# Kernel tuning notes

Hardware: AMD Instinct MI355X
Metric: run time of the kernel (lower is better)

## Reference

```python
import jax, jax.numpy as jnp
import numpy as np

N_EMITTERS = 200000
N_FRAMES = 500


def setup_inputs() -> dict:
    key = jax.random.key(0)
    k1, _ = jax.random.split(key)
    # initial state must be one-hot per emitter: column 0 = 'on', column 1 = 'off'
    on = jax.random.bernoulli(k1, 0.5, (N_EMITTERS,))
    initial = jnp.stack([on, ~on], axis=-1).astype(jnp.float32)  # [N, 2] one-hot
    # transition[j] is the categorical distribution over {stay-ish, flip-ish} given row j
    transition = jnp.array([[0.5, 0.5], [0.9, 0.1]], dtype=jnp.float32)
    # transition_matrix[0] = identity (keep state), transition_matrix[1] = swap (flip state)
    transition_matrix = jnp.array([[[1.0, 0.0], [0.0, 1.0]],
                                   [[0.0, 1.0], [1.0, 0.0]]], dtype=jnp.float32)
    return {"initial": initial, "transition": transition,
            "transition_matrix": transition_matrix, "n_frames": N_FRAMES}


def reference(initial, transition, transition_matrix, n_frames):
    # Faithful translation of the per-frame Python loop as a single lax.scan.
    # Original: A = Cat(transition).sample([N]) -> A[n, j] ~ Cat(transition[j, :]) in {0, 1}
    #           t = (state * A).sum(-1)   (selects A at the current one-hot state index)
    #           state = state @ transition_matrix[t]
    # Output: per-frame on-mask (original returned np.where(state[:, 0] == 1) indices,
    # which has data-dependent shape; we return the equivalent dense mask).
    p1 = transition[:, 1]  # prob of drawing class 1 for each of the 2 row-distributions
    keys = jax.random.split(jax.random.key(42), n_frames)

    def step(state, k):
        u = jax.random.uniform(k, (state.shape[0], 2), dtype=state.dtype)  # [N, 2]
        A = (u < p1[None, :]).astype(state.dtype)  # categorical sample per row dist, {0,1}
        t = jnp.sum(state * A, axis=-1).astype(jnp.int32)  # [N] chosen action per emitter
        m = transition_matrix[t]  # [N, 2, 2] identity-or-swap
        new_state = jnp.einsum('ni,nij->nj', state, m)  # [N, 2] one-hot update
        return new_state, new_state[:, 0]

    _, on_mask = jax.lax.scan(step, initial, keys)
    return on_mask  # [n_frames, N], 1.0 where emitter is in the 'on' state
```

## Files before the change

### kernel.cpp

```cpp
#include <hip/hip_runtime.h>
#include <stdint.h>


#define ROTL32(x, d) __builtin_amdgcn_alignbit((x), (x), 32 - (d))

typedef uint32_t v2u __attribute__((ext_vector_type(2)));

__device__ __forceinline__ void tf2x32(uint32_t k0, uint32_t k1,
                                       uint32_t x0, uint32_t x1,
                                       uint32_t& o0, uint32_t& o1) {
  const uint32_t k2 = k0 ^ k1 ^ 0x1BD11BDAu;
  x0 += k0; x1 += k1;
#define TF_R(d) { x0 += x1; x1 = ROTL32(x1, d) ^ x0; }
  TF_R(13) TF_R(15) TF_R(26) TF_R(6)
  x0 += k1; x1 += k2 + 1u;
  TF_R(17) TF_R(29) TF_R(16) TF_R(24)
  x0 += k2; x1 += k0 + 2u;
  TF_R(13) TF_R(15) TF_R(26) TF_R(6)
  x0 += k0; x1 += k1 + 3u;
  TF_R(17) TF_R(29) TF_R(16) TF_R(24)
  x0 += k1; x1 += k2 + 4u;
  TF_R(13) TF_R(15) TF_R(26) TF_R(6)
  x0 += k2; x1 += k0 + 5u;
#undef TF_R
  o0 = x0; o1 = x1;
}

__global__ void subkeys_kernel(uint2* __restrict__ ks, int nf, int cap) {
  const int f = blockIdx.x * blockDim.x + threadIdx.x;
  if (f < nf) {
    uint32_t a, b;
    tf2x32(0u, 42u, 0u, (uint32_t)f, a, b);
    ks[f] = make_uint2(a, b);
  } else if (f < cap) {
    ks[f] = make_uint2(0u, 0u);
  }
}

__device__ __forceinline__ v2u do_frame(
    uint32_t k0, uint32_t k1, uint32_t& sA, uint32_t& sB,
    uint32_t& thrA, uint32_t& thrB, uint32_t baseA, uint32_t baseB,
    uint32_t tsh0, uint32_t tsh1, uint32_t sw0, uint32_t sw1) {
  const uint32_t k2 = k0 ^ k1 ^ 0x1BD11BDAu;
  const uint32_t c1 = k2 + 1u, c2 = k0 + 2u, c3 = k1 + 3u,
                 c4 = k2 + 4u, c5 = k0 + 5u;

  uint32_t xa0 = k0, xa1 = baseA + sA + k1;
  uint32_t xb0 = k0, xb1 = baseB + sB + k1;

#define RND(d) { xa0 += xa1; xa1 = ROTL32(xa1, (d)) ^ xa0;   \
                 xb0 += xb1; xb1 = ROTL32(xb1, (d)) ^ xb0; }
  RND(13) RND(15) RND(26) RND(6)
  xa0 += k1; xa1 += c1; xb0 += k1; xb1 += c1;
  RND(17) RND(29) RND(16) RND(24)
  xa0 += k2; xa1 += c2; xb0 += k2; xb1 += c2;
  RND(13) RND(15) RND(26) RND(6)
  xa0 += k0; xa1 += c3; xb0 += k0; xb1 += c3;
  RND(17) RND(29) RND(16) RND(24)
  xa0 += k1; xa1 += c4; xb0 += k1; xb1 += c4;
  RND(13) RND(15) RND(26) RND(6)
  xa0 += k2; xa1 += c5; xb0 += k2; xb1 += c5;
#undef RND

  sA ^= ((xa0 ^ xa1) < thrA) ? sw1 : sw0;
  sB ^= ((xb0 ^ xb1) < thrB) ? sw1 : sw0;
  thrA = sA ? tsh1 : tsh0;
  thrB = sB ? tsh1 : tsh0;
  v2u v;
  v.x = sA ? 0u : 0x3f800000u;
  v.y = sB ? 0u : 0x3f800000u;
  return v;
}

__device__ __forceinline__ void markov_body(
    const float* __restrict__ initial, const float* __restrict__ transition,
    const float* __restrict__ tmat, const uint2* __restrict__ ks,
    float* __restrict__ out, int N, int nf) {
  const int t = blockIdx.x * blockDim.x + threadIdx.x;
  const int nA = 2 * t;
  const int nB = 2 * t + 1;
  if (nA >= N) return;
  const bool hasB = (nB < N);

  const uint64_t t0w = ((uint64_t)(uint32_t)ceilf(transition[1] * 8388608.0f)) << 9;
  const uint64_t t1w = ((uint64_t)(uint32_t)ceilf(transition[3] * 8388608.0f)) << 9;
  const uint32_t tsh0 = (t0w > 0xFFFFFFFFull) ? 0xFFFFFFFFu : (uint32_t)t0w;
  const uint32_t tsh1 = (t1w > 0xFFFFFFFFull) ? 0xFFFFFFFFu : (uint32_t)t1w;
  const uint32_t sw0 = (tmat[1] != 0.0f) ? 1u : 0u;
  const uint32_t sw1 = (tmat[5] != 0.0f) ? 1u : 0u;

  uint32_t sA = (initial[2 * nA] != 0.0f) ? 0u : 1u;
  uint32_t sB = hasB ? ((initial[2 * nB] != 0.0f) ? 0u : 1u) : 0u;
  uint32_t thrA = sA ? tsh1 : tsh0;
  uint32_t thrB = sB ? tsh1 : tsh0;
  const uint32_t baseA = 2u * (uint32_t)nA;
  const uint32_t baseB = 2u * (uint32_t)nB;

  float* op = out + nA;
  const uint4* kq = (const uint4*)ks;

  const int ng = nf / 4;
  uint4 a0 = kq[0], a1 = kq[1];
  if (hasB) {
    for (int g = 0; g < ng; ++g) {
      const uint4 b0 = kq[2 * g + 2];
      const uint4 b1 = kq[2 * g + 3];
      const v2u v0 = do_frame(a0.x, a0.y, sA, sB, thrA, thrB, baseA, baseB,
                              tsh0, tsh1, sw0, sw1);
      __builtin_nontemporal_store(v0, (v2u*)op); op += N;
      const v2u v1 = do_frame(a0.z, a0.w, sA, sB, thrA, thrB, baseA, baseB,
                              tsh0, tsh1, sw0, sw1);
      __builtin_nontemporal_store(v1, (v2u*)op); op += N;
      const v2u v2 = do_frame(a1.x, a1.y, sA, sB, thrA, thrB, baseA, baseB,
                              tsh0, tsh1, sw0, sw1);
      __builtin_nontemporal_store(v2, (v2u*)op); op += N;
      const v2u v3 = do_frame(a1.z, a1.w, sA, sB, thrA, thrB, baseA, baseB,
                              tsh0, tsh1, sw0, sw1);
      __builtin_nontemporal_store(v3, (v2u*)op); op += N;
      a0 = b0; a1 = b1;
    }
    for (int f = ng * 4; f < nf; ++f) {
      const uint2 k = ks[f];
      const v2u v = do_frame(k.x, k.y, sA, sB, thrA, thrB, baseA, baseB,
                             tsh0, tsh1, sw0, sw1);
      __builtin_nontemporal_store(v, (v2u*)op); op += N;
    }
  } else {
    for (int f = 0; f < nf; ++f) {
      const uint2 k = ks[f];
      const v2u v = do_frame(k.x, k.y, sA, sB, thrA, thrB, baseA, baseB,
                             tsh0, tsh1, sw0, sw1);
      __builtin_nontemporal_store(v.x, (uint32_t*)op); op += N;
    }
  }
}

__global__ __launch_bounds__(64) void markov_kernel(
    const float* __restrict__ initial, const float* __restrict__ transition,
    const float* __restrict__ tmat, const uint2* __restrict__ ks,
    float* __restrict__ out, int N, int nf) {
  markov_body(initial, transition, tmat, ks, out, N, nf);
}

__global__ __launch_bounds__(64) void markov_kernel_lds(
    const float* __restrict__ initial, const float* __restrict__ transition,
    const float* __restrict__ tmat, float* __restrict__ out,
    int N, int nf, int cap) {
  extern __shared__ uint2 kf[];
  for (int f = threadIdx.x; f < cap; f += blockDim.x) {
    uint2 k = make_uint2(0u, 0u);
    if (f < nf) {
      uint32_t a, b;
      tf2x32(0u, 42u, 0u, (uint32_t)f, a, b);
      k = make_uint2(a, b);
    }
    kf[f] = k;
  }
  __syncthreads();
  markov_body(initial, transition, tmat, kf, out, N, nf);
}

extern "C" void kernel_launch(void* const* d_in, const int* in_sizes, int n_in,
                              void* d_out, int out_size, void* d_ws, size_t ws_size,
                              hipStream_t stream) {
  const float* initial    = (const float*)d_in[0];
  const float* transition = (const float*)d_in[1];
  const float* tmat       = (const float*)d_in[2];
  float* out = (float*)d_out;

  const int N  = in_sizes[0] / 2;
  const int nf = (N > 0) ? (out_size / N) : 0;
  if (N <= 0 || nf <= 0) return;

  const int nthreads = (N + 1) / 2;
  const int block = 64;
  const int grid = (nthreads + block - 1) / block;

  const int cap = (nf / 4 + 2) * 4;
  const size_t need = (size_t)cap * sizeof(uint2);
  if (ws_size >= need) {
    uint2* ks = (uint2*)d_ws;
    subkeys_kernel<<<(cap + 255) / 256, 256, 0, stream>>>(ks, nf, cap);
    markov_kernel<<<grid, block, 0, stream>>>(initial, transition, tmat, ks,
                                              out, N, nf);
  } else {
    markov_kernel_lds<<<grid, block, need, stream>>>(initial, transition,
                                                     tmat, out, N, nf, cap);
  }
}
```

Measured before the change: 261.3 us.

## Process one emitter per thread with 256-thread blocks instead of two per thread

Each thread now handles a single emitter rather than a pair, which doubles the thread count (200k threads) and halves the per-thread ILP from two interleaved Threefry streams to one. Block size goes from 64 to 256 and output stores become 4-byte per lane instead of 8-byte vector stores. The goal is more wavefronts to hide latency and simpler code, at the cost of less per-thread instruction-level parallelism and twice as many subkey loads across the grid.

```diff
diff --git a/kernel.cpp b/kernel.cpp
--- a/kernel.cpp
+++ b/kernel.cpp
@@ -3,8 +3,6 @@
 
 
 #define ROTL32(x, d) __builtin_amdgcn_alignbit((x), (x), 32 - (d))
-
-typedef uint32_t v2u __attribute__((ext_vector_type(2)));
 
 __device__ __forceinline__ void tf2x32(uint32_t k0, uint32_t k1,
                                        uint32_t x0, uint32_t x1,
@@ -37,50 +35,38 @@
   }
 }
 
-__device__ __forceinline__ v2u do_frame(
-    uint32_t k0, uint32_t k1, uint32_t& sA, uint32_t& sB,
-    uint32_t& thrA, uint32_t& thrB, uint32_t baseA, uint32_t baseB,
+__device__ __forceinline__ uint32_t do_frame1(
+    uint32_t k0, uint32_t k1, uint32_t& s, uint32_t& thr, uint32_t base,
     uint32_t tsh0, uint32_t tsh1, uint32_t sw0, uint32_t sw1) {
   const uint32_t k2 = k0 ^ k1 ^ 0x1BD11BDAu;
   const uint32_t c1 = k2 + 1u, c2 = k0 + 2u, c3 = k1 + 3u,
                  c4 = k2 + 4u, c5 = k0 + 5u;
 
-  uint32_t xa0 = k0, xa1 = baseA + sA + k1;
-  uint32_t xb0 = k0, xb1 = baseB + sB + k1;
-
-#define RND(d) { xa0 += xa1; xa1 = ROTL32(xa1, (d)) ^ xa0;   \
-                 xb0 += xb1; xb1 = ROTL32(xb1, (d)) ^ xb0; }
+  uint32_t x0 = k0, x1 = base + s + k1;
+#define RND(d) { x0 += x1; x1 = ROTL32(x1, (d)) ^ x0; }
   RND(13) RND(15) RND(26) RND(6)
-  xa0 += k1; xa1 += c1; xb0 += k1; xb1 += c1;
+  x0 += k1; x1 += c1;
   RND(17) RND(29) RND(16) RND(24)
-  xa0 += k2; xa1 += c2; xb0 += k2; xb1 += c2;
+  x0 += k2; x1 += c2;
   RND(13) RND(15) RND(26) RND(6)
-  xa0 += k0; xa1 += c3; xb0 += k0; xb1 += c3;
+  x0 += k0; x1 += c3;
   RND(17) RND(29) RND(16) RND(24)
-  xa0 += k1; xa1 += c4; xb0 += k1; xb1 += c4;
+  x0 += k1; x1 += c4;
   RND(13) RND(15) RND(26) RND(6)
-  xa0 += k2; xa1 += c5; xb0 += k2; xb1 += c5;
+  x0 += k2; x1 += c5;
 #undef RND
 
-  sA ^= ((xa0 ^ xa1) < thrA) ? sw1 : sw0;
-  sB ^= ((xb0 ^ xb1) < thrB) ? sw1 : sw0;
-  thrA = sA ? tsh1 : tsh0;
-  thrB = sB ? tsh1 : tsh0;
-  v2u v;
-  v.x = sA ? 0u : 0x3f800000u;
-  v.y = sB ? 0u : 0x3f800000u;
-  return v;
+  s ^= ((x0 ^ x1) < thr) ? sw1 : sw0;
+  thr = s ? tsh1 : tsh0;
+  return s ? 0u : 0x3f800000u;
 }
 
 __device__ __forceinline__ void markov_body(
     const float* __restrict__ initial, const float* __restrict__ transition,
     const float* __restrict__ tmat, const uint2* __restrict__ ks,
     float* __restrict__ out, int N, int nf) {
-  const int t = blockIdx.x * blockDim.x + threadIdx.x;
-  const int nA = 2 * t;
-  const int nB = 2 * t + 1;
-  if (nA >= N) return;
-  const bool hasB = (nB < N);
+  const int n = blockIdx.x * blockDim.x + threadIdx.x;
+  if (n >= N) return;
 
   const uint64_t t0w = ((uint64_t)(uint32_t)ceilf(transition[1] * 8388608.0f)) << 9;
   const uint64_t t1w = ((uint64_t)(uint32_t)ceilf(transition[3] * 8388608.0f)) << 9;
@@ -89,60 +75,43 @@
   const uint32_t sw0 = (tmat[1] != 0.0f) ? 1u : 0u;
   const uint32_t sw1 = (tmat[5] != 0.0f) ? 1u : 0u;
 
-  uint32_t sA = (initial[2 * nA] != 0.0f) ? 0u : 1u;
-  uint32_t sB = hasB ? ((initial[2 * nB] != 0.0f) ? 0u : 1u) : 0u;
-  uint32_t thrA = sA ? tsh1 : tsh0;
-  uint32_t thrB = sB ? tsh1 : tsh0;
-  const uint32_t baseA = 2u * (uint32_t)nA;
-  const uint32_t baseB = 2u * (uint32_t)nB;
+  uint32_t s = (initial[2 * n] != 0.0f) ? 0u : 1u;
+  uint32_t thr = s ? tsh1 : tsh0;
+  const uint32_t base = 2u * (uint32_t)n;
 
-  float* op = out + nA;
+  uint32_t* op = (uint32_t*)(out + n);
   const uint4* kq = (const uint4*)ks;
 
   const int ng = nf / 4;
   uint4 a0 = kq[0], a1 = kq[1];
-  if (hasB) {
-    for (int g = 0; g < ng; ++g) {
-      const uint4 b0 = kq[2 * g + 2];
-      const uint4 b1 = kq[2 * g + 3];
-      const v2u v0 = do_frame(a0.x, a0.y, sA, sB, thrA, thrB, baseA, baseB,
-                              tsh0, tsh1, sw0, sw1);
-      __builtin_nontemporal_store(v0, (v2u*)op); op += N;
-      const v2u v1 = do_frame(a0.z, a0.w, sA, sB, thrA, thrB, baseA, baseB,
-                              tsh0, tsh1, sw0, sw1);
-      __builtin_nontemporal_store(v1, (v2u*)op); op += N;
-      const v2u v2 = do_frame(a1.x, a1.y, sA, sB, thrA, thrB, baseA, baseB,
-                              tsh0, tsh1, sw0, sw1);
-      __builtin_nontemporal_store(v2, (v2u*)op); op += N;
-      const v2u v3 = do_frame(a1.z, a1.w, sA, sB, thrA, thrB, baseA, baseB,
-                              tsh0, tsh1, sw0, sw1);
-      __builtin_nontemporal_store(v3, (v2u*)op); op += N;
-      a0 = b0; a1 = b1;
-    }
-    for (int f = ng * 4; f < nf; ++f) {
-      const uint2 k = ks[f];
-      const v2u v = do_frame(k.x, k.y, sA, sB, thrA, thrB, baseA, baseB,
-                             tsh0, tsh1, sw0, sw1);
-      __builtin_nontemporal_store(v, (v2u*)op); op += N;
-    }
-  } else {
-    for (int f = 0; f < nf; ++f) {
-      const uint2 k = ks[f];
-      const v2u v = do_frame(k.x, k.y, sA, sB, thrA, thrB, baseA, baseB,
-                             tsh0, tsh1, sw0, sw1);
-      __builtin_nontemporal_store(v.x, (uint32_t*)op); op += N;
-    }
+  for (int g = 0; g < ng; ++g) {
+    const uint4 b0 = kq[2 * g + 2];
+    const uint4 b1 = kq[2 * g + 3];
+    const uint32_t v0 = do_frame1(a0.x, a0.y, s, thr, base, tsh0, tsh1, sw0, sw1);
+    __builtin_nontemporal_store(v0, op); op += N;
+    const uint32_t v1 = do_frame1(a0.z, a0.w, s, thr, base, tsh0, tsh1, sw0, sw1);
+    __builtin_nontemporal_store(v1, op); op += N;
+    const uint32_t v2 = do_frame1(a1.x, a1.y, s, thr, base, tsh0, tsh1, sw0, sw1);
+    __builtin_nontemporal_store(v2, op); op += N;
+    const uint32_t v3 = do_frame1(a1.z, a1.w, s, thr, base, tsh0, tsh1, sw0, sw1);
+    __builtin_nontemporal_store(v3, op); op += N;
+    a0 = b0; a1 = b1;
+  }
+  for (int f = ng * 4; f < nf; ++f) {
+    const uint2 k = ks[f];
+    const uint32_t v = do_frame1(k.x, k.y, s, thr, base, tsh0, tsh1, sw0, sw1);
+    __builtin_nontemporal_store(v, op); op += N;
   }
 }
 
-__global__ __launch_bounds__(64) void markov_kernel(
+__global__ __launch_bounds__(256) void markov_kernel(
     const float* __restrict__ initial, const float* __restrict__ transition,
     const float* __restrict__ tmat, const uint2* __restrict__ ks,
     float* __restrict__ out, int N, int nf) {
   markov_body(initial, transition, tmat, ks, out, N, nf);
 }
 
-__global__ __launch_bounds__(64) void markov_kernel_lds(
+__global__ __launch_bounds__(256) void markov_kernel_lds(
     const float* __restrict__ initial, const float* __restrict__ transition,
     const float* __restrict__ tmat, float* __restrict__ out,
     int N, int nf, int cap) {
@@ -172,9 +141,8 @@
   const int nf = (N > 0) ? (out_size / N) : 0;
   if (N <= 0 || nf <= 0) return;
 
-  const int nthreads = (N + 1) / 2;
-  const int block = 64;
-  const int grid = (nthreads + block - 1) / block;
+  const int block = 256;
+  const int grid = (N + block - 1) / block;
 
   const int cap = (nf / 4 + 2) * 4;
   const size_t need = (size_t)cap * sizeof(uint2);
```

New measurement: 278.4 us. 1.07x slower.
